# Kernel optimization log

Hardware: AMD Instinct MI355X
Metric: run time of the kernel (lower is better)

The kernel has to match this reference:

```python
import jax, jax.numpy as jnp
import numpy as np

B, C = 16384, 1000

def setup_inputs() -> dict:
    key = jax.random.key(0)
    k1, k2, k3 = jax.random.split(key, 3)
    out = jax.random.normal(k1, (B, C), dtype=jnp.float32)
    target = jax.random.randint(k2, (B,), 0, C, dtype=jnp.int64)
    # noise transition matrix: positive entries (row-normalization not required by the math)
    T = jax.random.uniform(k3, (C, C), dtype=jnp.float32)
    return {"out": out, "target": target, "T": T}

def reference(out, target, T):
    # softmax probabilities and log-probs, each computed once for the whole batch
    p = jax.nn.softmax(out, axis=1)            # [B, C]
    logp = jax.nn.log_softmax(out, axis=1)     # [B, C]
    idx = jnp.arange(out.shape[0])
    pro1 = p[idx, target]                      # p_i[y_i]
    # torch: (T.t() @ p_i.t()).t()[:, y_i] == (p_i @ T)[y_i]
    pro2 = (p @ T)[idx, target]                # [B]
    # beta is wrapped in a fresh Variable in torch -> no grad flows through it
    beta = jax.lax.stop_gradient(pro1 / pro2)
    ce = -logp[idx, target]                    # per-sample cross entropy
    # reduction='sum' (default)
    return jnp.sum(beta * ce)
```

## Files before the change

### kernel.cpp

```cpp
#include <hip/hip_runtime.h>
#include <math.h>

#define C 1000
#define C4 250

__device__ __forceinline__ float wave_reduce_max(float v) {
#pragma unroll
  for (int off = 32; off > 0; off >>= 1) v = fmaxf(v, __shfl_xor(v, off, 64));
  return v;
}
__device__ __forceinline__ float wave_reduce_sum(float v) {
#pragma unroll
  for (int off = 32; off > 0; off >>= 1) v += __shfl_xor(v, off, 64);
  return v;
}

__global__ __launch_bounds__(256) void transpose_zero_k(
    const float* __restrict__ A, float* __restrict__ At,
    float* __restrict__ result, int do_transpose) {
  if (blockIdx.x == 0 && blockIdx.y == 0 && threadIdx.x == 0 && threadIdx.y == 0)
    *result = 0.0f;
  if (!do_transpose) return;
  __shared__ float tile[32][33];
  int x = blockIdx.x * 32 + threadIdx.x;
#pragma unroll
  for (int k = 0; k < 32; k += 8) {
    int y = blockIdx.y * 32 + threadIdx.y + k;
    if (x < C && y < C) tile[threadIdx.y + k][threadIdx.x] = A[(size_t)y * C + x];
  }
  __syncthreads();
  int xt = blockIdx.y * 32 + threadIdx.x;
#pragma unroll
  for (int k = 0; k < 32; k += 8) {
    int yt = blockIdx.x * 32 + threadIdx.y + k;
    if (xt < C && yt < C) At[(size_t)yt * C + xt] = tile[threadIdx.x][threadIdx.y + k];
  }
}

__global__ __launch_bounds__(256) void reweight_k(
    const float* __restrict__ xin, const int* __restrict__ target,
    const float* __restrict__ Tmat, int tt_mode,
    float* __restrict__ partial, float* __restrict__ result, int B) {
  int wid = threadIdx.x >> 6;
  int lane = threadIdx.x & 63;
  int row = blockIdx.x * 4 + wid;
  float contrib = 0.0f;
  if (row < B) {
    const float4* x4 = (const float4*)(xin + (size_t)row * C);
    int y = target[row];
    float4 v[4];
    float m = -INFINITY;
#pragma unroll
    for (int k = 0; k < 4; k++) {
      int j = lane + k * 64;
      if (j < C4) {
        v[k] = x4[j];
        m = fmaxf(m, fmaxf(fmaxf(v[k].x, v[k].y), fmaxf(v[k].z, v[k].w)));
      }
    }
    m = wave_reduce_max(m);
    float se = 0.0f, st = 0.0f;
    if (tt_mode) {
      const float4* t4 = (const float4*)(Tmat + (size_t)y * C);
#pragma unroll
      for (int k = 0; k < 4; k++) {
        int j = lane + k * 64;
        if (j < C4) {
          float4 t = t4[j];
          float e0 = __expf(v[k].x - m), e1 = __expf(v[k].y - m);
          float e2 = __expf(v[k].z - m), e3 = __expf(v[k].w - m);
          se += (e0 + e1) + (e2 + e3);
          st += e0 * t.x + e1 * t.y + e2 * t.z + e3 * t.w;
        }
      }
    } else {
#pragma unroll
      for (int k = 0; k < 4; k++) {
        int j = lane + k * 64;
        if (j < C4) {
          int jb = j * 4;
          float e0 = __expf(v[k].x - m), e1 = __expf(v[k].y - m);
          float e2 = __expf(v[k].z - m), e3 = __expf(v[k].w - m);
          se += (e0 + e1) + (e2 + e3);
          st += e0 * Tmat[(size_t)(jb + 0) * C + y] +
                e1 * Tmat[(size_t)(jb + 1) * C + y] +
                e2 * Tmat[(size_t)(jb + 2) * C + y] +
                e3 * Tmat[(size_t)(jb + 3) * C + y];
        }
      }
    }
    se = wave_reduce_sum(se);
    st = wave_reduce_sum(st);
    if (lane == 0) {
      float xy = xin[(size_t)row * C + y];
      float ey = __expf(xy - m);
      float ce = logf(se) - (xy - m);
      contrib = (ey / st) * ce;
    }
  }
  __shared__ float bsum[4];
  if (lane == 0) bsum[wid] = contrib;
  __syncthreads();
  if (threadIdx.x == 0) {
    float s = (bsum[0] + bsum[1]) + (bsum[2] + bsum[3]);
    if (partial) partial[blockIdx.x] = s;
    else atomicAdd(result, s);
  }
}

__global__ __launch_bounds__(256) void reduce_k(const float* __restrict__ partial,
                                                float* __restrict__ result, int n) {
  float s = 0.0f;
  for (int i = threadIdx.x; i < n; i += 256) s += partial[i];
  s = wave_reduce_sum(s);
  __shared__ float b[4];
  if ((threadIdx.x & 63) == 0) b[threadIdx.x >> 6] = s;
  __syncthreads();
  if (threadIdx.x == 0) *result = (b[0] + b[1]) + (b[2] + b[3]);
}

extern "C" void kernel_launch(void* const* d_in, const int* in_sizes, int n_in,
                              void* d_out, int out_size, void* d_ws, size_t ws_size,
                              hipStream_t stream) {
  const float* xin = (const float*)d_in[0];
  const int* target = (const int*)d_in[1];
  const float* T = (const float*)d_in[2];
  float* result = (float*)d_out;
  int B = in_sizes[1];
  int nblocks = (B + 3) / 4;

  size_t tt_bytes = (size_t)C * C * sizeof(float);
  size_t need = tt_bytes + (size_t)nblocks * sizeof(float);

  if (ws_size >= need) {
    float* Tt = (float*)d_ws;
    float* partial = (float*)((char*)d_ws + tt_bytes);
    transpose_zero_k<<<dim3(32, 32), dim3(32, 8), 0, stream>>>(T, Tt, result, 1);
    reweight_k<<<nblocks, 256, 0, stream>>>(xin, target, Tt, 1, partial, result, B);
    reduce_k<<<1, 256, 0, stream>>>(partial, result, nblocks);
  } else {
    transpose_zero_k<<<dim3(32, 32), dim3(32, 8), 0, stream>>>(T, nullptr, result, 0);
    reweight_k<<<nblocks, 256, 0, stream>>>(xin, target, T, 0, nullptr, result, B);
  }
}
```

Before: 106.0 us.

## Fuse transpose, reweight and reduction into one cooperative persistent kernel

Replaces the three launches (T transpose, per-row reweight, final reduce) with a single cooperative kernel of 1024 blocks that transposes T, grid-syncs, processes rows in a grid-stride loop and reduces the per-block partials after a second grid sync. The aim is to remove two kernel launches and the gaps between them, and to issue the T-row loads alongside the logit loads. In exchange it adds two grid-wide barriers and requires all 1024 blocks to be co-resident. The 1024-block grid also caps parallelism for the 16384 rows.

New measurement: 304.2 us. +187.0%, slower.

```diff
diff --git a/kernel.cpp b/kernel.cpp
--- a/kernel.cpp
+++ b/kernel.cpp
@@ -1,8 +1,14 @@
 #include <hip/hip_runtime.h>
+#include <hip/hip_cooperative_groups.h>
 #include <math.h>
+
+namespace cg = cooperative_groups;
 
 #define C 1000
 #define C4 250
+#define NBLK 1024
+#define NTHR 256
+#define NWAVE (NBLK * 4)
 
 __device__ __forceinline__ float wave_reduce_max(float v) {
 #pragma unroll
@@ -14,6 +20,89 @@
   for (int off = 32; off > 0; off >>= 1) v += __shfl_xor(v, off, 64);
   return v;
 }
+
+__global__ __launch_bounds__(NTHR, 4) void fused_k(
+    const float* __restrict__ xin, const int* __restrict__ target,
+    const float* __restrict__ Tin, float* __restrict__ Tt,
+    float* __restrict__ partial, float* __restrict__ result, int B) {
+  __shared__ float tile[32][33];
+  __shared__ float bsum[4];
+  cg::grid_group grid = cg::this_grid();
+
+  {
+    int tx = (blockIdx.x & 31) << 5;
+    int ty = (blockIdx.x >> 5) << 5;
+    int lx = threadIdx.x & 31;
+    int ly = threadIdx.x >> 5;
+#pragma unroll
+    for (int k = 0; k < 32; k += 8) {
+      int x = tx + lx, y = ty + ly + k;
+      if (x < C && y < C) tile[ly + k][lx] = Tin[(size_t)y * C + x];
+    }
+    __syncthreads();
+#pragma unroll
+    for (int k = 0; k < 32; k += 8) {
+      int xt = ty + lx, yt = tx + ly + k;
+      if (xt < C && yt < C) Tt[(size_t)yt * C + xt] = tile[lx][ly + k];
+    }
+  }
+  grid.sync();
+
+  int wid = threadIdx.x >> 6;
+  int lane = threadIdx.x & 63;
+  int gw = blockIdx.x * 4 + wid;
+  float acc = 0.0f;
+  for (int row = gw; row < B; row += NWAVE) {
+    const float4* x4 = (const float4*)(xin + (size_t)row * C);
+    int y = target[row];
+    const float4* t4 = (const float4*)(Tt + (size_t)y * C);
+    float4 v[4], t[4];
+    float m = -INFINITY;
+#pragma unroll
+    for (int k = 0; k < 4; k++) {
+      int j = lane + k * 64;
+      if (j < C4) {
+        v[k] = x4[j];
+        t[k] = t4[j];
+        m = fmaxf(m, fmaxf(fmaxf(v[k].x, v[k].y), fmaxf(v[k].z, v[k].w)));
+      }
+    }
+    m = wave_reduce_max(m);
+    float se = 0.0f, st = 0.0f;
+#pragma unroll
+    for (int k = 0; k < 4; k++) {
+      int j = lane + k * 64;
+      if (j < C4) {
+        float e0 = __expf(v[k].x - m), e1 = __expf(v[k].y - m);
+        float e2 = __expf(v[k].z - m), e3 = __expf(v[k].w - m);
+        se += (e0 + e1) + (e2 + e3);
+        st += e0 * t[k].x + e1 * t[k].y + e2 * t[k].z + e3 * t[k].w;
+      }
+    }
+    se = wave_reduce_sum(se);
+    st = wave_reduce_sum(st);
+    if (lane == 0) {
+      float xy = xin[(size_t)row * C + y];
+      float ey = __expf(xy - m);
+      acc += (ey / st) * (logf(se) - (xy - m));
+    }
+  }
+  if (lane == 0) bsum[wid] = acc;
+  __syncthreads();
+  if (threadIdx.x == 0)
+    partial[blockIdx.x] = (bsum[0] + bsum[1]) + (bsum[2] + bsum[3]);
+  grid.sync();
+
+  if (blockIdx.x == 0) {
+    float s = 0.0f;
+    for (int i = threadIdx.x; i < NBLK; i += NTHR) s += partial[i];
+    s = wave_reduce_sum(s);
+    if (lane == 0) bsum[wid] = s;
+    __syncthreads();
+    if (threadIdx.x == 0) *result = (bsum[0] + bsum[1]) + (bsum[2] + bsum[3]);
+  }
+}
+
 
 __global__ __launch_bounds__(256) void transpose_zero_k(
     const float* __restrict__ A, float* __restrict__ At,
@@ -108,17 +197,6 @@
   }
 }
 
-__global__ __launch_bounds__(256) void reduce_k(const float* __restrict__ partial,
-                                                float* __restrict__ result, int n) {
-  float s = 0.0f;
-  for (int i = threadIdx.x; i < n; i += 256) s += partial[i];
-  s = wave_reduce_sum(s);
-  __shared__ float b[4];
-  if ((threadIdx.x & 63) == 0) b[threadIdx.x >> 6] = s;
-  __syncthreads();
-  if (threadIdx.x == 0) *result = (b[0] + b[1]) + (b[2] + b[3]);
-}
-
 extern "C" void kernel_launch(void* const* d_in, const int* in_sizes, int n_in,
                               void* d_out, int out_size, void* d_ws, size_t ws_size,
                               hipStream_t stream) {
@@ -127,18 +205,25 @@
   const float* T = (const float*)d_in[2];
   float* result = (float*)d_out;
   int B = in_sizes[1];
-  int nblocks = (B + 3) / 4;
 
   size_t tt_bytes = (size_t)C * C * sizeof(float);
-  size_t need = tt_bytes + (size_t)nblocks * sizeof(float);
+  size_t need = tt_bytes + (size_t)NBLK * sizeof(float);
 
   if (ws_size >= need) {
     float* Tt = (float*)d_ws;
     float* partial = (float*)((char*)d_ws + tt_bytes);
-    transpose_zero_k<<<dim3(32, 32), dim3(32, 8), 0, stream>>>(T, Tt, result, 1);
-    reweight_k<<<nblocks, 256, 0, stream>>>(xin, target, Tt, 1, partial, result, B);
-    reduce_k<<<1, 256, 0, stream>>>(partial, result, nblocks);
+    void* args[7];
+    args[0] = (void*)&xin;
+    args[1] = (void*)&target;
+    args[2] = (void*)&T;
+    args[3] = (void*)&Tt;
+    args[4] = (void*)&partial;
+    args[5] = (void*)&result;
+    args[6] = (void*)&B;
+    hipLaunchCooperativeKernel((const void*)fused_k, dim3(NBLK), dim3(NTHR),
+                               args, 0, stream);
   } else {
+    int nblocks = (B + 3) / 4;
     transpose_zero_k<<<dim3(32, 32), dim3(32, 8), 0, stream>>>(T, nullptr, result, 0);
     reweight_k<<<nblocks, 256, 0, stream>>>(xin, target, T, 0, nullptr, result, B);
   }
```
